# Kernel optimization log

Measured on AMD Instinct MI355X. Metric: run time of the kernel, lower is better.

## Reference

```python
import jax, jax.numpy as jnp
import numpy as np

NUM_EMBEDDINGS = 1024
EMBEDDING_DIM = 32  # Z_NH
COMMITMENT_LOSS_FACTOR = 0.1
QUANTIZATION_LOSS_FACTOR = 0.1


def setup_inputs() -> dict:
    key = jax.random.key(0)
    k1, k2 = jax.random.split(key)
    h = jax.random.normal(k1, (256, 512, EMBEDDING_DIM), dtype=jnp.float32)
    # nn.Embedding weight init: uniform(-1/K, 1/K)
    embeddings = jax.random.uniform(
        k2, (NUM_EMBEDDINGS, EMBEDDING_DIM), dtype=jnp.float32,
        minval=-1.0 / NUM_EMBEDDINGS, maxval=1.0 / NUM_EMBEDDINGS)
    return {"h": h, "embeddings": embeddings}


def reference(h, embeddings):
    flat = h.reshape(-1, EMBEDDING_DIM)                       # [N, D]
    dist = ((flat ** 2).sum(-1, keepdims=True)
            + (embeddings ** 2).sum(-1)
            - 2.0 * flat @ embeddings.T)                      # [N, K]
    idx = jnp.argmin(dist, axis=-1)                           # [N]
    # one_hot @ weight == direct row gather
    quantized = embeddings[idx].reshape(h.shape)              # [B, S, D]
    q_flat = quantized.reshape(-1, EMBEDDING_DIM)
    commitment_loss = jnp.mean((jax.lax.stop_gradient(q_flat) - flat) ** 2, axis=-1)
    embedding_loss = jnp.mean((q_flat - jax.lax.stop_gradient(flat)) ** 2, axis=-1)
    # straight-through estimator
    quantized_st = h + jax.lax.stop_gradient(quantized - h)
    loss = (commitment_loss * COMMITMENT_LOSS_FACTOR
            + embedding_loss * QUANTIZATION_LOSS_FACTOR)      # [N]
    quantized_indices = idx[:, None]                          # [N, 1]
    return quantized_st, quantized_indices, loss
```

## Files before the change

kernel.cpp:

```cpp
#include <hip/hip_runtime.h>


#define EMB_N 1024
#define DIM 32
#define NVEC (256 * 512)
#define NTILES (EMB_N / 16)
#define MAXC 8

typedef unsigned long long u64;
typedef unsigned int u32;
typedef unsigned short ushortT;
typedef __attribute__((ext_vector_type(8))) short bf16x8;
typedef __attribute__((ext_vector_type(4))) float f32x4;

__device__ __forceinline__ u32 enc_f32(float x) {
    u32 u = __float_as_uint(x);
    return (u & 0x80000000u) ? ~u : (u | 0x80000000u);
}
__device__ __forceinline__ ushortT f2bf(float f) {
    u32 u = __float_as_uint(f);
    return (ushortT)((u + 0x7FFFu + ((u >> 16) & 1u)) >> 16);
}
__device__ __forceinline__ u64 shflx_u64(u64 x, int m) {
    int lo = __shfl_xor((int)(u32)x, m);
    int hi = __shfl_xor((int)(x >> 32), m);
    return ((u64)(u32)hi << 32) | (u32)lo;
}

__device__ __forceinline__ float norm2_np(const float* fr) {
    float sq[DIM];
#pragma unroll
    for (int i = 0; i < DIM; ++i) sq[i] = fr[i] * fr[i];
    float r[8];
#pragma unroll
    for (int j = 0; j < 8; ++j)
        r[j] = ((sq[j] + sq[j + 8]) + sq[j + 16]) + sq[j + 24];
    return ((r[0] + r[1]) + (r[2] + r[3])) + ((r[4] + r[5]) + (r[6] + r[7]));
}

__global__ __launch_bounds__(256) void prep_kernel(
    const float* __restrict__ emb, float* __restrict__ e2,
    ushortT* __restrict__ bfrag)
{
#pragma clang fp contract(off)
    const int t = blockIdx.x * 256 + threadIdx.x;
    const int l = t & 63;
    const int row = ((t >> 6) << 4) + (l & 15);
    const int k0 = (l >> 4) * 8;
    const float* ep = emb + (size_t)row * DIM + k0;
    ushortT* dst = bfrag + (size_t)t * 8;
#pragma unroll
    for (int j = 0; j < 8; ++j) dst[j] = f2bf(ep[j]);
    if (t < EMB_N) {
        const float* e = emb + (size_t)t * DIM;
        float tmp[DIM];
#pragma unroll
        for (int i = 0; i < DIM; ++i) tmp[i] = e[i];
        e2[t] = norm2_np(tmp);
    }
}

__global__ __launch_bounds__(256) void vq_scan(
    const float* __restrict__ h,
    const float* __restrict__ emb,
    const float* __restrict__ e2,
    const ushortT* __restrict__ bfrag,
    float* __restrict__ out_q, float* __restrict__ out_idx,
    float* __restrict__ out_loss)
{
#pragma clang fp contract(off)
    __shared__ u32 lds_cnt[4][32];
    __shared__ u32 lds_cand[4][32 * MAXC];

    const int wslot = threadIdx.x >> 6;
    const int wid   = (blockIdx.x * 256 + threadIdx.x) >> 6;
    const int lane  = threadIdx.x & 63;
    const int col16 = lane & 15;
    const int quad  = lane >> 4;
    const size_t row0 = (size_t)wid * 32;

    u32* cnt  = lds_cnt[wslot];
    u32* cand = lds_cand[wslot];
    if (lane < 32) cnt[lane] = 0;

    bf16x8 afr0, afr1;
    float sa0, sa1;
    {
        const float* ap = h + (row0 + col16) * DIM + quad * 8;
        float4 x = *(const float4*)ap, y = *(const float4*)(ap + 4);
        afr0[0]=(short)f2bf(x.x); afr0[1]=(short)f2bf(x.y); afr0[2]=(short)f2bf(x.z); afr0[3]=(short)f2bf(x.w);
        afr0[4]=(short)f2bf(y.x); afr0[5]=(short)f2bf(y.y); afr0[6]=(short)f2bf(y.z); afr0[7]=(short)f2bf(y.w);
        sa0 = fabsf(x.x)+fabsf(x.y)+fabsf(x.z)+fabsf(x.w)+fabsf(y.x)+fabsf(y.y)+fabsf(y.z)+fabsf(y.w);
        const float* bp = ap + 16 * DIM;
        float4 u = *(const float4*)bp, v = *(const float4*)(bp + 4);
        afr1[0]=(short)f2bf(u.x); afr1[1]=(short)f2bf(u.y); afr1[2]=(short)f2bf(u.z); afr1[3]=(short)f2bf(u.w);
        afr1[4]=(short)f2bf(v.x); afr1[5]=(short)f2bf(v.y); afr1[6]=(short)f2bf(v.z); afr1[7]=(short)f2bf(v.w);
        sa1 = fabsf(u.x)+fabsf(u.y)+fabsf(u.z)+fabsf(u.w)+fabsf(v.x)+fabsf(v.y)+fabsf(v.z)+fabsf(v.w);
    }
    sa0 += __shfl_xor(sa0, 16); sa0 += __shfl_xor(sa0, 32);
    sa1 += __shfl_xor(sa1, 16); sa1 += __shfl_xor(sa1, 32);

    const f32x4 zacc = {0.f, 0.f, 0.f, 0.f};

    float bs[8];
#pragma unroll
    for (int i = 0; i < 8; ++i) bs[i] = 3.4e38f;
#pragma unroll 2
    for (int nt = 0; nt < NTILES; ++nt) {
        bf16x8 b = *(const bf16x8*)(bfrag + nt * 512 + lane * 8);
        f32x4 d0 = __builtin_amdgcn_mfma_f32_16x16x32_bf16(afr0, b, zacc, 0, 0, 0);
        f32x4 d1 = __builtin_amdgcn_mfma_f32_16x16x32_bf16(afr1, b, zacc, 0, 0, 0);
        float e2c = e2[nt * 16 + col16];
#pragma unroll
        for (int r = 0; r < 4; ++r) {
            bs[r]     = fminf(bs[r],     __builtin_fmaf(-2.f, d0[r], e2c));
            bs[4 + r] = fminf(bs[4 + r], __builtin_fmaf(-2.f, d1[r], e2c));
        }
    }
#pragma unroll
    for (int m = 1; m < 16; m <<= 1)
#pragma unroll
        for (int i = 0; i < 8; ++i) bs[i] = fminf(bs[i], __shfl_xor(bs[i], m));

    float thr[8];
#pragma unroll
    for (int i = 0; i < 8; ++i) {
        float sar = __shfl((i >> 2) ? sa1 : sa0, quad * 4 + (i & 3));
        thr[i] = bs[i] + __builtin_fmaf(sar, 0x1p-16f, 1.0e-4f);
    }

#pragma unroll 2
    for (int nt = 0; nt < NTILES; ++nt) {
        bf16x8 b = *(const bf16x8*)(bfrag + nt * 512 + lane * 8);
        f32x4 d0 = __builtin_amdgcn_mfma_f32_16x16x32_bf16(afr0, b, zacc, 0, 0, 0);
        f32x4 d1 = __builtin_amdgcn_mfma_f32_16x16x32_bf16(afr1, b, zacc, 0, 0, 0);
        float e2c = e2[nt * 16 + col16];
        const u32 cc = nt * 16 + col16;
        bool q[8];
        bool any = false;
#pragma unroll
        for (int i = 0; i < 8; ++i) {
            float s = __builtin_fmaf(-2.f, ((i >> 2) ? d1[i & 3] : d0[i & 3]), e2c);
            q[i] = (s <= thr[i]);
            any |= q[i];
        }
        if (__ballot(any)) {
#pragma unroll
            for (int i = 0; i < 8; ++i) {
                if (__ballot(q[i])) {
                    if (q[i]) {
                        const int rloc = ((i >> 2) << 4) + quad * 4 + (i & 3);
                        u32 slot = atomicAdd(&cnt[rloc], 1u);
                        if (slot < MAXC) cand[rloc * MAXC + slot] = cc;
                    }
                }
            }
        }
    }

    u64 ovf = __ballot((lane < 32) && (cnt[lane & 31] > MAXC));
    while (ovf) {
        const int r = (int)(__ffsll((unsigned long long)ovf) - 1);
        ovf &= ovf - 1;
        const float* fp = h + (row0 + r) * DIM;
        float fu[DIM];
#pragma unroll
        for (int i = 0; i < DIM; i += 4) {
            float4 x = *(const float4*)(fp + i);
            fu[i] = x.x; fu[i + 1] = x.y; fu[i + 2] = x.z; fu[i + 3] = x.w;
        }
        const float f2 = norm2_np(fu);
        u64 bk = ~0ull;
        for (int c = lane; c < EMB_N; c += 64) {
            const float* ep = emb + (size_t)c * DIM;
            float a = 0.f;
#pragma unroll
            for (int k = 0; k < DIM; ++k) a = __builtin_fmaf(fu[k], ep[k], a);
            float dd = (f2 + e2[c]) - (2.0f * a);
            u64 key = ((u64)enc_f32(dd) << 32) | (u32)c;
            if (key < bk) bk = key;
        }
#pragma unroll
        for (int m = 1; m < 64; m <<= 1) {
            u64 o = shflx_u64(bk, m);
            if (o < bk) bk = o;
        }
        if (lane == 0) { cand[r * MAXC] = (u32)bk; cnt[r] = 1; }
    }

    if (lane < 32) {
        const int row = (int)row0 + lane;
        const u32 n = cnt[lane];
        const float* f = h + (size_t)row * DIM;
        float fr[DIM];
#pragma unroll
        for (int i = 0; i < DIM; i += 4) {
            float4 x = *(const float4*)(f + i);
            fr[i] = x.x; fr[i + 1] = x.y; fr[i + 2] = x.z; fr[i + 3] = x.w;
        }
        int bidx;
        if (n == 1) {
            bidx = (int)cand[lane * MAXC];
        } else {
            const float f2 = norm2_np(fr);
            u64 best = ~0ull;
            for (u32 j = 0; j < n; ++j) {
                const u32 c = cand[lane * MAXC + j];
                const float* ep = emb + (size_t)c * DIM;
                float a = 0.f;
#pragma unroll
                for (int k = 0; k < DIM; ++k) a = __builtin_fmaf(fr[k], ep[k], a);
                float dd = (f2 + e2[c]) - (2.0f * a);
                u64 key = ((u64)enc_f32(dd) << 32) | c;
                if (key < best) best = key;
            }
            bidx = (int)(best & 0xFFFFFFFFu);
        }

        const float* qv = emb + (size_t)bidx * DIM;
        float ps = 0.f;
#pragma unroll
        for (int i = 0; i < DIM; i += 4) {
            float4 qx; qx.x = qv[i]; qx.y = qv[i+1]; qx.z = qv[i+2]; qx.w = qv[i+3];
            float dx = qx.x - fr[i], dy = qx.y - fr[i+1], dz = qx.z - fr[i+2], dw = qx.w - fr[i+3];
            ps += dx * dx; ps += dy * dy; ps += dz * dz; ps += dw * dw;
            float4 o;
            o.x = fr[i]     + (qx.x - fr[i]);
            o.y = fr[i + 1] + (qx.y - fr[i + 1]);
            o.z = fr[i + 2] + (qx.z - fr[i + 2]);
            o.w = fr[i + 3] + (qx.w - fr[i + 3]);
            *(float4*)(out_q + (size_t)row * DIM + i) = o;
        }
        float m = ps * (1.0f / DIM);
        out_idx[row]  = (float)bidx;
        out_loss[row] = m * 0.1f + m * 0.1f;
    }
}

__global__ void e2_kernel(const float* __restrict__ emb, float* __restrict__ e2) {
#pragma clang fp contract(off)
    int c = blockIdx.x * blockDim.x + threadIdx.x;
    if (c >= EMB_N) return;
    const float* e = emb + (size_t)c * DIM;
    float tmp[DIM];
#pragma unroll
    for (int i = 0; i < DIM; ++i) tmp[i] = e[i];
    e2[c] = norm2_np(tmp);
}

__global__ __launch_bounds__(256) void vq_kernel(
    const float* __restrict__ h, const float* __restrict__ emb,
    const float* __restrict__ e2, float* __restrict__ out_q,
    float* __restrict__ out_idx, float* __restrict__ out_loss)
{
#pragma clang fp contract(off)
    const int v = blockIdx.x * blockDim.x + threadIdx.x;
    const float* f = h + (size_t)v * DIM;
    float fr[DIM];
#pragma unroll
    for (int i = 0; i < DIM; i += 4) {
        float4 x = *(const float4*)(f + i);
        fr[i] = x.x; fr[i + 1] = x.y; fr[i + 2] = x.z; fr[i + 3] = x.w;
    }
    const float f2 = norm2_np(fr);
    float best = 3.4e38f; int bidx = 0;
#pragma unroll 1
    for (int c = 0; c < EMB_N; ++c) {
        const float* e = emb + (size_t)c * DIM;
        float a0 = 0.f;
#pragma unroll
        for (int k = 0; k < DIM; ++k) a0 = __builtin_fmaf(fr[k], e[k], a0);
        float d0 = (f2 + e2[c]) - (2.0f * a0);
        if (d0 < best) { best = d0; bidx = c; }
    }
    const float* q = emb + (size_t)bidx * DIM;
    float ps = 0.f;
#pragma unroll
    for (int i = 0; i < DIM; i += 4) {
        float4 qx; qx.x = q[i]; qx.y = q[i+1]; qx.z = q[i+2]; qx.w = q[i+3];
        float dx = qx.x - fr[i], dy = qx.y - fr[i+1], dz = qx.z - fr[i+2], dw = qx.w - fr[i+3];
        ps += dx * dx; ps += dy * dy; ps += dz * dz; ps += dw * dw;
        float4 o;
        o.x = fr[i] + (qx.x - fr[i]); o.y = fr[i+1] + (qx.y - fr[i+1]);
        o.z = fr[i+2] + (qx.z - fr[i+2]); o.w = fr[i+3] + (qx.w - fr[i+3]);
        *(float4*)(out_q + (size_t)v * DIM + i) = o;
    }
    float m = ps * (1.0f / DIM);
    out_idx[v]  = (float)bidx;
    out_loss[v] = m * 0.1f + m * 0.1f;
}

extern "C" void kernel_launch(void* const* d_in, const int* in_sizes, int n_in,
                              void* d_out, int out_size, void* d_ws, size_t ws_size,
                              hipStream_t stream) {
    const float* h   = (const float*)d_in[0];
    const float* emb = (const float*)d_in[1];
    float* out = (float*)d_out;
    float* out_q    = out;
    float* out_idx  = out + (size_t)NVEC * DIM;
    float* out_loss = out + (size_t)NVEC * DIM + NVEC;

    float*   e2    = (float*)d_ws;
    ushortT* bfrag = (ushortT*)((char*)d_ws + 4096);
    const size_t need = 4096 + (size_t)NTILES * 512 * sizeof(ushortT);

    if (ws_size >= need) {
        prep_kernel<<<16, 256, 0, stream>>>(emb, e2, bfrag);
        vq_scan<<<1024, 256, 0, stream>>>(h, emb, e2, bfrag, out_q, out_idx, out_loss);
    } else {
        e2_kernel<<<EMB_N / 256, 256, 0, stream>>>(emb, e2);
        vq_kernel<<<NVEC / 256, 256, 0, stream>>>(h, emb, e2, out_q, out_idx, out_loss);
    }
}
```

Measured before the change: 131.2 us.

## Stage bf16 codebook fragments in LDS and keep candidates in registers

```diff
diff --git a/kernel.cpp b/kernel.cpp
--- a/kernel.cpp
+++ b/kernel.cpp
@@ -5,7 +5,7 @@
 #define DIM 32
 #define NVEC (256 * 512)
 #define NTILES (EMB_N / 16)
-#define MAXC 8
+#define MAXC 6
 
 typedef unsigned long long u64;
 typedef unsigned int u32;
@@ -69,19 +69,20 @@
     float* __restrict__ out_loss)
 {
 #pragma clang fp contract(off)
-    __shared__ u32 lds_cnt[4][32];
-    __shared__ u32 lds_cand[4][32 * MAXC];
-
-    const int wslot = threadIdx.x >> 6;
+    __shared__ __align__(16) ushortT s_b[EMB_N * DIM];
+
+    {
+        const uint4* src = (const uint4*)bfrag;
+        uint4* dst = (uint4*)s_b;
+#pragma unroll 4
+        for (int o = threadIdx.x; o < 4096; o += 256) dst[o] = src[o];
+    }
+
     const int wid   = (blockIdx.x * 256 + threadIdx.x) >> 6;
     const int lane  = threadIdx.x & 63;
     const int col16 = lane & 15;
     const int quad  = lane >> 4;
     const size_t row0 = (size_t)wid * 32;
-
-    u32* cnt  = lds_cnt[wslot];
-    u32* cand = lds_cand[wslot];
-    if (lane < 32) cnt[lane] = 0;
 
     bf16x8 afr0, afr1;
     float sa0, sa1;
@@ -100,6 +101,8 @@
     sa0 += __shfl_xor(sa0, 16); sa0 += __shfl_xor(sa0, 32);
     sa1 += __shfl_xor(sa1, 16); sa1 += __shfl_xor(sa1, 32);
 
+    __syncthreads();
+
     const f32x4 zacc = {0.f, 0.f, 0.f, 0.f};
 
     float bs[8];
@@ -107,7 +110,7 @@
     for (int i = 0; i < 8; ++i) bs[i] = 3.4e38f;
 #pragma unroll 2
     for (int nt = 0; nt < NTILES; ++nt) {
-        bf16x8 b = *(const bf16x8*)(bfrag + nt * 512 + lane * 8);
+        bf16x8 b = *(const bf16x8*)(s_b + nt * 512 + lane * 8);
         f32x4 d0 = __builtin_amdgcn_mfma_f32_16x16x32_bf16(afr0, b, zacc, 0, 0, 0);
         f32x4 d1 = __builtin_amdgcn_mfma_f32_16x16x32_bf16(afr1, b, zacc, 0, 0, 0);
         float e2c = e2[nt * 16 + col16];
@@ -129,13 +132,16 @@
         thr[i] = bs[i] + __builtin_fmaf(sar, 0x1p-16f, 1.0e-4f);
     }
 
+    u64 packed = 0;
+    u32 nreal  = 0;
+    const int i_r = ((lane >> 4) << 2) | (lane & 3);
+    const int g_sh = ((lane >> 2) & 3) * 16;
 #pragma unroll 2
     for (int nt = 0; nt < NTILES; ++nt) {
-        bf16x8 b = *(const bf16x8*)(bfrag + nt * 512 + lane * 8);
+        bf16x8 b = *(const bf16x8*)(s_b + nt * 512 + lane * 8);
         f32x4 d0 = __builtin_amdgcn_mfma_f32_16x16x32_bf16(afr0, b, zacc, 0, 0, 0);
         f32x4 d1 = __builtin_amdgcn_mfma_f32_16x16x32_bf16(afr1, b, zacc, 0, 0, 0);
         float e2c = e2[nt * 16 + col16];
-        const u32 cc = nt * 16 + col16;
         bool q[8];
         bool any = false;
 #pragma unroll
@@ -144,21 +150,33 @@
             q[i] = (s <= thr[i]);
             any |= q[i];
         }
-        if (__ballot(any)) {
-#pragma unroll
-            for (int i = 0; i < 8; ++i) {
-                if (__ballot(q[i])) {
-                    if (q[i]) {
-                        const int rloc = ((i >> 2) << 4) + quad * 4 + (i & 3);
-                        u32 slot = atomicAdd(&cnt[rloc], 1u);
-                        if (slot < MAXC) cand[rloc * MAXC + slot] = cc;
-                    }
+        if (__any(any)) {
+            u64 B0 = __ballot(q[0]), B1 = __ballot(q[1]);
+            u64 B2 = __ballot(q[2]), B3 = __ballot(q[3]);
+            u64 B4 = __ballot(q[4]), B5 = __ballot(q[5]);
+            u64 B6 = __ballot(q[6]), B7 = __ballot(q[7]);
+            if (lane < 32) {
+                u64 s01 = (i_r & 1) ? B1 : B0;
+                u64 s23 = (i_r & 1) ? B3 : B2;
+                u64 s45 = (i_r & 1) ? B5 : B4;
+                u64 s67 = (i_r & 1) ? B7 : B6;
+                u64 t0  = (i_r & 2) ? s23 : s01;
+                u64 t1  = (i_r & 2) ? s67 : s45;
+                u64 sel = (i_r & 4) ? t1 : t0;
+                u32 fld = (u32)(sel >> g_sh) & 0xFFFFu;
+                while (fld) {
+                    int bit = __ffs(fld) - 1;
+                    fld &= fld - 1;
+                    u32 c = (u32)(nt * 16 + bit);
+                    if (nreal < MAXC) packed |= (u64)c << (nreal * 10);
+                    ++nreal;
                 }
             }
         }
     }
 
-    u64 ovf = __ballot((lane < 32) && (cnt[lane & 31] > MAXC));
+    int myBidx = -1;
+    u64 ovf = __ballot((lane < 32) && (nreal > MAXC));
     while (ovf) {
         const int r = (int)(__ffsll((unsigned long long)ovf) - 1);
         ovf &= ovf - 1;
@@ -185,12 +203,11 @@
             u64 o = shflx_u64(bk, m);
             if (o < bk) bk = o;
         }
-        if (lane == 0) { cand[r * MAXC] = (u32)bk; cnt[r] = 1; }
+        if (lane == r) myBidx = (int)(bk & 0xFFFFFFFFu);
     }
 
     if (lane < 32) {
         const int row = (int)row0 + lane;
-        const u32 n = cnt[lane];
         const float* f = h + (size_t)row * DIM;
         float fr[DIM];
 #pragma unroll
@@ -199,13 +216,15 @@
             fr[i] = x.x; fr[i + 1] = x.y; fr[i + 2] = x.z; fr[i + 3] = x.w;
         }
         int bidx;
-        if (n == 1) {
-            bidx = (int)cand[lane * MAXC];
+        if (myBidx >= 0) {
+            bidx = myBidx;
+        } else if (nreal == 1) {
+            bidx = (int)(packed & 1023u);
         } else {
             const float f2 = norm2_np(fr);
             u64 best = ~0ull;
-            for (u32 j = 0; j < n; ++j) {
-                const u32 c = cand[lane * MAXC + j];
+            for (u32 j = 0; j < nreal; ++j) {
+                const u32 c = (u32)((packed >> (j * 10)) & 1023u);
                 const float* ep = emb + (size_t)c * DIM;
                 float a = 0.f;
 #pragma unroll
@@ -302,11 +321,12 @@
 
     float*   e2    = (float*)d_ws;
     ushortT* bfrag = (ushortT*)((char*)d_ws + 4096);
-    const size_t need = 4096 + (size_t)NTILES * 512 * sizeof(ushortT);
+    const size_t need = 4096 + (size_t)EMB_N * DIM * sizeof(ushortT);
 
     if (ws_size >= need) {
         prep_kernel<<<16, 256, 0, stream>>>(emb, e2, bfrag);
-        vq_scan<<<1024, 256, 0, stream>>>(h, emb, e2, bfrag, out_q, out_idx, out_loss);
+        vq_scan<<<1024, 256, 0, stream>>>(h, emb, e2, bfrag,
+                                          out_q, out_idx, out_loss);
     } else {
         e2_kernel<<<EMB_N / 256, 256, 0, stream>>>(emb, e2);
         vq_kernel<<<NVEC / 256, 256, 0, stream>>>(h, emb, e2, out_q, out_idx, out_loss);
```

Result: slower. 149.4 us (+13.8%).
